# Optimization experiments

Measured on AMD Instinct MI355X. Metric: run time of the kernel, lower is better.

The kernel has to match this reference:

```python
import jax, jax.numpy as jnp
import numpy as np

C = 256
BN_EPS = 1e-5


def conv1x1(x, w, b):
    # x: (B, Cin, H, W), w: (Cout, Cin), b: (Cout,)
    return jnp.einsum('bchw,oc->bohw', x, w) + b[None, :, None, None]


def setup_inputs() -> dict:
    key = jax.random.key(0)
    ks = jax.random.split(key, 12)
    B, H, W = 8, 64, 64
    s = 1.0 / np.sqrt(C)
    inp = {
        'xi': jax.random.normal(ks[0], (B, C, H, W), jnp.float32),
        'xj': jax.random.normal(ks[1], (B, C, H, W), jnp.float32),
        'g_w': jax.random.normal(ks[2], (C, C), jnp.float32) * s,
        'g_b': jax.random.normal(ks[3], (C,), jnp.float32) * s,
        'theta_w': jax.random.normal(ks[4], (C, C), jnp.float32) * s,
        'theta_b': jax.random.normal(ks[5], (C,), jnp.float32) * s,
        'phi_w': jax.random.normal(ks[6], (C, C), jnp.float32) * s,
        'phi_b': jax.random.normal(ks[7], (C,), jnp.float32) * s,
        'W_w': jax.random.normal(ks[8], (C, C), jnp.float32) * s,
        'W_b': jax.random.normal(ks[9], (C,), jnp.float32) * s,
        'bn_gamma': jnp.ones((C,), jnp.float32),
        'bn_beta': jnp.zeros((C,), jnp.float32),
    }
    return inp


def reference(xi, xj, g_w, g_b, theta_w, theta_b, phi_w, phi_b, W_w, W_b, bn_gamma, bn_beta):
    B, Cc, H, W = xi.shape
    N = H * W
    # 1x1 conv projections, flattened to token sequences
    g_x = conv1x1(xj, g_w, g_b).reshape(B, Cc, N)        # (B, C, N)
    theta_x = conv1x1(xi, theta_w, theta_b).reshape(B, Cc, N)  # (B, C, N)
    phi_x = conv1x1(xj, phi_w, phi_b).reshape(B, Cc, N)  # (B, C, N)
    # f = theta^T @ phi, scaled by N (no softmax)
    f = jnp.einsum('bcn,bcm->bnm', theta_x, phi_x) / N   # (B, N, N)
    # y = f @ g^T, back to channel-first
    y = jnp.einsum('bnm,bcm->bcn', f, g_x).reshape(B, Cc, H, W)
    W_y = conv1x1(y, W_w, W_b)
    z = W_y + xi
    # BatchNorm2d (training-mode batch statistics, biased variance)
    mean = jnp.mean(z, axis=(0, 2, 3), keepdims=True)
    var = jnp.var(z, axis=(0, 2, 3), keepdims=True)
    z_hat = (z - mean) * jax.lax.rsqrt(var + BN_EPS)
    return z_hat * bn_gamma[None, :, None, None] + bn_beta[None, :, None, None]
```

## Files before the change

kernel.cpp:

```cpp
#include <hip/hip_runtime.h>
#include <cstddef>

#define CCH 256
#define NPIX 4096
#define NB 8
#define INVCNT (1.0f/32768.0f)
#define INVN (1.0f/4096.0f)

typedef __bf16 bf16_t;
typedef __attribute__((ext_vector_type(8))) __bf16 bf16x8;
typedef __attribute__((ext_vector_type(4))) __bf16 bf16x4;
typedef __attribute__((ext_vector_type(4))) float f32x4;

#define OFF_S      0u
#define OFF_AB     2048u
#define OFF_BMT    34816u
#define OFF_T1     67584u
#define OFF_R      67840u
#define OFF_W1     68096u
#define OFF_C1     68352u
#define OFF_G      68608u
#define OFF_MP     330752u
#define OFF_E      592896u
#define OFF_RSP    594944u
#define OFF_ZPS    627712u
#define OFF_ZPQ    758784u
#define OFF_SCALE  889856u
#define OFF_SHIFT  890112u
#define OFF_GP     890368u
#define OFF_XIT    5084672u

__device__ __forceinline__ void pack8(const float4& x, const float4& y, bf16x8& o) {
  o[0]=(bf16_t)x.x; o[1]=(bf16_t)x.y; o[2]=(bf16_t)x.z; o[3]=(bf16_t)x.w;
  o[4]=(bf16_t)y.x; o[5]=(bf16_t)y.y; o[6]=(bf16_t)y.z; o[7]=(bf16_t)y.w;
}

__device__ __forceinline__ void ld4(const float* p, float4& a0, float4& a1, float4& a2, float4& a3) {
  a0 = *(const float4*)p;       a1 = *(const float4*)(p + 4);
  a2 = *(const float4*)(p + 8); a3 = *(const float4*)(p + 12);
}

template <bool ATRANS>
__device__ __forceinline__ void mm64v(const float* __restrict__ A,
                                      const float* __restrict__ B,
                                      int i0, int j0,
                                      float (&acc)[2][4],
                                      float (*s1)[65], float (*s2)[65]) {
  const int t = threadIdx.x, tx = t & 15, ty = t >> 4;
  for (int k0 = 0; k0 < 256; k0 += 64) {
#pragma unroll
    for (int it = 0; it < 2; ++it) {
      const int f = t + 512 * it;
      const int row = f >> 4, cc = (f & 15) * 4;
      float4 va;
      if (ATRANS)
        va = *(const float4*)(A + (size_t)(k0 + row) * CCH + i0 + cc);
      else
        va = *(const float4*)(A + (size_t)(i0 + row) * CCH + k0 + cc);
      const float4 vb = *(const float4*)(B + (size_t)(k0 + row) * CCH + j0 + cc);
      s1[row][cc + 0] = va.x; s1[row][cc + 1] = va.y; s1[row][cc + 2] = va.z; s1[row][cc + 3] = va.w;
      s2[row][cc + 0] = vb.x; s2[row][cc + 1] = vb.y; s2[row][cc + 2] = vb.z; s2[row][cc + 3] = vb.w;
    }
    __syncthreads();
#pragma unroll 4
    for (int kk = 0; kk < 64; ++kk) {
      float ar[2], br[4];
#pragma unroll
      for (int i = 0; i < 2; ++i) ar[i] = ATRANS ? s1[kk][2 * ty + i] : s1[2 * ty + i][kk];
#pragma unroll
      for (int j = 0; j < 4; ++j) br[j] = s2[kk][4 * tx + j];
#pragma unroll
      for (int i = 0; i < 2; ++i)
#pragma unroll
        for (int j = 0; j < 4; ++j) acc[i][j] += ar[i] * br[j];
    }
    __syncthreads();
  }
}

__device__ void pre_body(int blk, const float* Ww, const float* gw, const float* phw,
                         const float* thw, const float* gb, const float* phb,
                         const float* thb, float* ws, unsigned char* SMEM) {
  const int t = threadIdx.x;
  if (blk < 32) {
    float (*s1)[65] = (float(*)[65])SMEM;
    float (*s2)[65] = (float(*)[65])(SMEM + 16640);
    const int tb = blk & 15;
    const int i0 = (tb >> 2) * 64, j0 = (tb & 3) * 64;
    float acc[2][4] = {};
    if (blk < 16) mm64v<false>(Ww, gw, i0, j0, acc, s1, s2);
    else          mm64v<true >(thw, phw, i0, j0, acc, s1, s2);
    bf16_t* outp = (bf16_t*)(ws + (blk < 16 ? OFF_AB : OFF_BMT));
    const int tx = t & 15, ty = t >> 4;
#pragma unroll
    for (int i = 0; i < 2; ++i) {
      bf16x4 mv;
#pragma unroll
      for (int q = 0; q < 4; ++q) mv[q] = (bf16_t)acc[i][q];
      *(bf16x4*)&outp[(size_t)(i0 + 2 * ty + i) * CCH + j0 + 4 * tx] = mv;
    }
  } else {
    if (t < 256) {
      float t1v = 0.f, rv = 0.f, w1v = 0.f;
      for (int k = 0; k < 256; ++k) {
        t1v += phw[k * CCH + t] * thb[k];
        rv  += thw[k * CCH + t] * phb[k];
        w1v += Ww[t * CCH + k] * gb[k];
      }
      ws[OFF_T1 + t] = t1v; ws[OFF_R + t] = rv; ws[OFF_W1 + t] = w1v;
    }
    float* red = (float*)SMEM;
    red[t] = (t < 256) ? phb[t] * thb[t] : 0.f;
    __syncthreads();
    for (int off = 256; off; off >>= 1) { if (t < off) red[t] += red[t + off]; __syncthreads(); }
    if (t == 0) ws[OFF_C1] = red[0];
  }
}

__device__ void cvtT_body(int bx, int b, const float* __restrict__ xi,
                          float* __restrict__ ws, unsigned char* SMEM) {
  bf16_t (*st)[72] = (bf16_t(*)[72])SMEM;
  const int c0 = (bx & 1) * 128;
  const int n0 = (bx >> 1) * 64;
  const float* X = xi + (size_t)b * CCH * NPIX;
  const int t = threadIdx.x;
  const int r = t >> 2, c4 = (t & 3) * 16;
  {
    float4 a0, a1, a2, a3;
    ld4(X + (size_t)(c0 + r) * NPIX + n0 + c4, a0, a1, a2, a3);
    bf16x8 u0, u1;
    pack8(a0, a1, u0); pack8(a2, a3, u1);
    *(bf16x8*)&st[r][c4] = u0;
    *(bf16x8*)&st[r][c4 + 8] = u1;
  }
  __syncthreads();
  bf16_t* Xit = (bf16_t*)(ws + OFF_XIT) + (size_t)b * NPIX * CCH;
  const int nr = t >> 3, cc = (t & 7) * 16;
  bf16x8 o0, o1;
#pragma unroll
  for (int j = 0; j < 8; ++j) o0[j] = st[cc + j][nr];
#pragma unroll
  for (int j = 0; j < 8; ++j) o1[j] = st[cc + 8 + j][nr];
  *(bf16x8*)(Xit + (size_t)(n0 + nr) * CCH + c0 + cc) = o0;
  *(bf16x8*)(Xit + (size_t)(n0 + nr) * CCH + c0 + cc + 8) = o1;
}

__device__ void gram_body(int ks, int b, const float* __restrict__ X,
                          float* __restrict__ ws, unsigned char* SMEM) {
  bf16_t (*sA)[256][40] = (bf16_t(*)[256][40])SMEM;
  const int t = threadIdx.x;
  const int w = t >> 6, lane = t & 63;
  const int wr = w >> 1, wc = w & 1;
  const int lr = lane & 15, hi = lane >> 4;
  const int fcol = 8 * hi;
  const f32x4 z4 = {0.f, 0.f, 0.f, 0.f};
  f32x4 acc[4][8];
#pragma unroll
  for (int fr = 0; fr < 4; ++fr)
#pragma unroll
    for (int fc = 0; fc < 8; ++fc) acc[fr][fc] = z4;
  float rsum = 0.f;
  const int k0 = ks * 256;
  const int srow = t >> 1, sh16 = (t & 1) * 16;

  float4 a0, a1, a2, a3;
  auto LOAD = [&](int kc) {
    ld4(X + (size_t)srow * NPIX + k0 + kc + sh16, a0, a1, a2, a3);
    rsum += a0.x + a0.y + a0.z + a0.w + a1.x + a1.y + a1.z + a1.w
          + a2.x + a2.y + a2.z + a2.w + a3.x + a3.y + a3.z + a3.w;
  };
  auto WRITE = [&](int q) {
    bf16x8 u0, u1;
    pack8(a0, a1, u0); pack8(a2, a3, u1);
    *(bf16x8*)&sA[q][srow][sh16] = u0;
    *(bf16x8*)&sA[q][srow][sh16 + 8] = u1;
  };

  LOAD(0);
  WRITE(0);
  __syncthreads();
  int cur = 0;
  for (int kc8 = 0; kc8 < 8; ++kc8) {
    if (kc8 < 7) LOAD(32 * (kc8 + 1));
    bf16x8 af[4];
#pragma unroll
    for (int fr = 0; fr < 4; ++fr)
      af[fr] = *(const bf16x8*)&sA[cur][64 * wr + 16 * fr + lr][fcol];
#pragma unroll
    for (int fc = 0; fc < 8; ++fc) {
      const bf16x8 bv = *(const bf16x8*)&sA[cur][128 * wc + 16 * fc + lr][fcol];
#pragma unroll
      for (int fr = 0; fr < 4; ++fr)
        acc[fr][fc] = __builtin_amdgcn_mfma_f32_16x16x32_bf16(af[fr], bv, acc[fr][fc], 0, 0, 0);
    }
    if (kc8 < 7) WRITE(cur ^ 1);
    __syncthreads();
    cur ^= 1;
  }

  {
    const float o = __shfl_down(rsum, 1);
    if (!(t & 1)) ws[OFF_RSP + ((size_t)(b * 16 + ks)) * CCH + srow] = rsum + o;
  }
  bf16_t* GPp = (bf16_t*)(ws + OFF_GP) + (size_t)(b * 16 + ks) * 65536;
  bf16_t (*sT)[264] = (bf16_t(*)[264])SMEM;
  const int rl = 16 * wr + 4 * hi;
#pragma unroll
  for (int fr = 0; fr < 4; ++fr) {
    __syncthreads();
#pragma unroll
    for (int fc = 0; fc < 8; ++fc)
#pragma unroll
      for (int reg = 0; reg < 4; ++reg)
        sT[rl + reg][128 * wc + 16 * fc + lr] = (bf16_t)acc[fr][fc][reg];
    __syncthreads();
    const int row = t >> 3;
    const int c32 = (t & 7) * 32;
    const int grow = 64 * (row >> 4) + 16 * fr + (row & 15);
#pragma unroll
    for (int q = 0; q < 4; ++q) {
      const bf16x8 v = *(const bf16x8*)&sT[row][c32 + 8 * q];
      *(bf16x8*)&GPp[(size_t)grow * CCH + c32 + 8 * q] = v;
    }
  }
}

__global__ __launch_bounds__(512) void k_mega(const float* __restrict__ xi,
                                              const float* __restrict__ xj,
                                              const float* __restrict__ Ww,
                                              const float* __restrict__ gw,
                                              const float* __restrict__ phw,
                                              const float* __restrict__ thw,
                                              const float* __restrict__ gb,
                                              const float* __restrict__ phb,
                                              const float* __restrict__ thb,
                                              float* __restrict__ ws) {
  __shared__ __align__(16) unsigned char SMEM[40960];
  const int bx = blockIdx.x, by = blockIdx.y;
  if (bx >= 144) {
    if (by == 0) pre_body(bx - 144, Ww, gw, phw, thw, gb, phb, thb, ws, SMEM);
    return;
  }
  if (bx >= 16) { cvtT_body(bx - 16, by, xi, ws, SMEM); return; }
  gram_body(bx, by, xj + (size_t)by * CCH * NPIX, ws, SMEM);
}

__global__ __launch_bounds__(256) void k_greduce(float* __restrict__ ws) {
  const int b = blockIdx.y, bx = blockIdx.x, t = threadIdx.x;
  const bf16_t* GPp = (const bf16_t*)(ws + OFF_GP) + (size_t)b * 16 * 65536;
  bf16_t* Gb = (bf16_t*)(ws + OFF_G) + (size_t)b * 65536;
  const int row = bx * 8 + (t >> 5);
  const int j8 = (t & 31) * 8;
  float s[8] = {};
#pragma unroll
  for (int ks = 0; ks < 16; ++ks) {
    const bf16x8 v = *(const bf16x8*)&GPp[(size_t)ks * 65536 + row * CCH + j8];
#pragma unroll
    for (int q = 0; q < 8; ++q) s[q] += (float)v[q];
  }
  bf16x8 o;
#pragma unroll
  for (int q = 0; q < 8; ++q) o[q] = (bf16_t)s[q];
  *(bf16x8*)&Gb[(size_t)row * CCH + j8] = o;
  if (t < 128) {
    const int rr = bx * 8 + (t >> 4), l = t & 15;
    float v = ws[OFF_RSP + ((size_t)(b * 16 + l)) * CCH + rr];
#pragma unroll
    for (int off = 8; off; off >>= 1) v += __shfl_down(v, off, 16);
    if (l == 0) ws[OFF_S + b * CCH + rr] = v;
  }
}

__global__ __launch_bounds__(256) void k_kmmat(const float* __restrict__ Wb, float* __restrict__ ws) {
  const int b = blockIdx.y;
  const int i0 = blockIdx.x * 32;
  const int t = threadIdx.x;
  const int w = t >> 6, lane = t & 63;
  const int rg = w >> 1, cg = w & 1;
  const int lr = lane & 15, hi = lane >> 4;
  const int fcol = 8 * hi;

  __shared__ __align__(16) bf16_t sA[2][32][40];
  __shared__ __align__(16) bf16_t sB[2][256][40];
  __shared__ __align__(16) bf16_t sK[32][264];
  __shared__ float sS[256], sT1[256], sR[256], sW1[256], sVS[256];
  __shared__ float sU[32];
  __shared__ float red[256];
  __shared__ float sdt_sh;

  const bf16_t* Ab  = (const bf16_t*)(ws + OFF_AB);
  const bf16_t* BmT = (const bf16_t*)(ws + OFF_BMT);
  const bf16_t* Gb  = (const bf16_t*)(ws + OFF_G) + (size_t)b * 65536;

  sS[t]  = ws[OFF_S + b * CCH + t];
  sT1[t] = ws[OFF_T1 + t];
  sR[t]  = ws[OFF_R + t];
  sW1[t] = ws[OFF_W1 + t];
  __syncthreads();
  red[t] = sS[t] * sT1[t];
  __syncthreads();
  for (int off = 128; off; off >>= 1) { if (t < off) red[t] += red[t + off]; __syncthreads(); }
  if (t == 0) sdt_sh = red[0];
  {
    float a = 0.f;
    for (int k8 = 0; k8 < 256; k8 += 8) {
      const bf16x8 v = *(const bf16x8*)&BmT[(size_t)t * CCH + k8];
#pragma unroll
      for (int q = 0; q < 8; ++q) a += (float)v[q] * sS[k8 + q];
    }
    sVS[t] = a;
  }
  if (t < 32) {
    float a = 0.f;
    for (int k8 = 0; k8 < 256; k8 += 8) {
      const bf16x8 v = *(const bf16x8*)&Ab[(size_t)(i0 + t) * CCH + k8];
#pragma unroll
      for (int q = 0; q < 8; ++q) a += (float)v[q] * sS[k8 + q];
    }
    sU[t] = a;
  }

  const f32x4 z4 = {0.f, 0.f, 0.f, 0.f};
  const int arow = t >> 2, achk = (t & 3) * 8;

  f32x4 acc[8];
#pragma unroll
  for (int fc = 0; fc < 8; ++fc) acc[fc] = z4;
  bf16x8 ra;
  bf16x8 gb8[4];
  auto LOADB = [&](int k) {
    if (t < 128) ra = *(const bf16x8*)&Ab[(size_t)(i0 + arow) * CCH + k + achk];
#pragma unroll
    for (int h = 0; h < 4; ++h)
      gb8[h] = *(const bf16x8*)&Gb[(size_t)(64 * h + arow) * CCH + k + achk];
  };
  auto WRITEB = [&](int q) {
    if (t < 128) *(bf16x8*)&sA[q][arow][achk] = ra;
#pragma unroll
    for (int h = 0; h < 4; ++h)
      *(bf16x8*)&sB[q][64 * h + arow][achk] = gb8[h];
  };
  LOADB(0);
  WRITEB(0);
  __syncthreads();
  int cur = 0;
  for (int ks = 0; ks < 8; ++ks) {
    if (ks < 7) LOADB(32 * (ks + 1));
    const bf16x8 af = *(const bf16x8*)&sA[cur][16 * rg + lr][fcol];
#pragma unroll
    for (int fc = 0; fc < 8; ++fc) {
      const bf16x8 bv = *(const bf16x8*)&sB[cur][128 * cg + 16 * fc + lr][fcol];
      acc[fc] = __builtin_amdgcn_mfma_f32_16x16x32_bf16(af, bv, acc[fc], 0, 0, 0);
    }
    if (ks < 7) WRITEB(cur ^ 1);
    __syncthreads();
    cur ^= 1;
  }
#pragma unroll
  for (int fc = 0; fc < 8; ++fc)
#pragma unroll
    for (int reg = 0; reg < 4; ++reg)
      sK[16 * rg + 4 * hi + reg][128 * cg + 16 * fc + lr] = (bf16_t)acc[fc][reg];
  __syncthreads();

  if (t < 32) {
    float dot = 0.f;
    for (int k8 = 0; k8 < 256; k8 += 8) {
      const bf16x8 v = *(const bf16x8*)&sK[t][k8];
#pragma unroll
      for (int q = 0; q < 8; ++q) dot += (float)v[q] * sT1[k8 + q];
    }
    const float c1 = ws[OFF_C1];
    const float ui = sU[t], w1i = sW1[i0 + t];
    ws[OFF_E + b * CCH + i0 + t] = INVN * (dot + c1 * ui + sdt_sh * w1i) + c1 * w1i + Wb[i0 + t];
  }

  f32x4 acc2[8];
#pragma unroll
  for (int fc = 0; fc < 8; ++fc) acc2[fc] = z4;
  bf16x8 rb[4];
  auto LOADC = [&](int k) {
#pragma unroll
    for (int h = 0; h < 4; ++h)
      rb[h] = *(const bf16x8*)&BmT[(size_t)(64 * h + arow) * CCH + k + achk];
  };
  auto WRITEC = [&](int q) {
#pragma unroll
    for (int h = 0; h < 4; ++h)
      *(bf16x8*)&sB[q][64 * h + arow][achk] = rb[h];
  };
  LOADC(0);
  WRITEC(0);
  __syncthreads();
  cur = 0;
  for (int ks = 0; ks < 8; ++ks) {
    if (ks < 7) LOADC(32 * (ks + 1));
    const bf16x8 af = *(const bf16x8*)&sK[16 * rg + lr][32 * ks + fcol];
#pragma unroll
    for (int fc = 0; fc < 8; ++fc) {
      const bf16x8 bv = *(const bf16x8*)&sB[cur][128 * cg + 16 * fc + lr][fcol];
      acc2[fc] = __builtin_amdgcn_mfma_f32_16x16x32_bf16(af, bv, acc2[fc], 0, 0, 0);
    }
    if (ks < 7) WRITEC(cur ^ 1);
    __syncthreads();
    cur ^= 1;
  }

  bf16_t* Mp = (bf16_t*)(ws + OFF_MP) + (size_t)b * 65536;
#pragma unroll
  for (int fc = 0; fc < 8; ++fc) {
    const int j = 128 * cg + 16 * fc + lr;
    const float rj = sR[j], vsj = sVS[j];
#pragma unroll
    for (int reg = 0; reg < 4; ++reg) {
      const int il = 16 * rg + 4 * hi + reg;
      const float ui = sU[il], w1i = sW1[i0 + il];
      float m = (acc2[fc][reg] + ui * rj + w1i * vsj) * INVN + w1i * rj;
      if (i0 + il == j) m += 1.0f;
      sK[16 * rg + 4 * hi + reg][128 * cg + 16 * fc + lr] = (bf16_t)m;
    }
  }
  __syncthreads();
  {
    const int row = t >> 3;
    const int c32 = (t & 7) * 32;
#pragma unroll
    for (int q = 0; q < 4; ++q) {
      const bf16x8 v = *(const bf16x8*)&sK[row][c32 + 8 * q];
      *(bf16x8*)&Mp[(size_t)(i0 + row) * CCH + c32 + 8 * q] = v;
    }
  }
}

template <int APPLY>
__global__ __launch_bounds__(256) void k_zmm(float* __restrict__ ws, float* __restrict__ out) {
  const int b = blockIdx.y, nblk = blockIdx.x;
  const int n0 = nblk * 64;
  const int t = threadIdx.x;
  const int w = t >> 6, lane = t & 63;
  const int rg = w >> 1, cg = w & 1;
  __shared__ __align__(16) bf16_t sA[2][64][40];
  __shared__ __align__(16) bf16_t sB[2][256][40];
  __shared__ float sC1[256], sC2[256];
  __shared__ float redS[4][128], redQ[4][128];
  {
    const float e = ws[OFF_E + b * CCH + t];
    if (APPLY) {
      const float sc = ws[OFF_SCALE + t];
      sC1[t] = sc;
      sC2[t] = e * sc + ws[OFF_SHIFT + t];
    } else {
      sC1[t] = e;
    }
  }
  const bf16_t* Xit = (const bf16_t*)(ws + OFF_XIT) + (size_t)b * NPIX * CCH;
  const bf16_t* Mp = (const bf16_t*)(ws + OFF_MP) + (size_t)b * 65536;
  const f32x4 z4 = {0.f, 0.f, 0.f, 0.f};
  f32x4 acc[2][8];
#pragma unroll
  for (int fr = 0; fr < 2; ++fr)
#pragma unroll
    for (int fc = 0; fc < 8; ++fc) acc[fr][fc] = z4;
  const int arow = t >> 2, achk = (t & 3) * 8;
  bf16x8 ra, rb0, rb1, rb2, rb3;
  ra  = *(const bf16x8*)(Xit + (size_t)(n0 + arow) * CCH + achk);
  rb0 = *(const bf16x8*)(Mp + (size_t)(arow)       * CCH + achk);
  rb1 = *(const bf16x8*)(Mp + (size_t)(64 + arow)  * CCH + achk);
  rb2 = *(const bf16x8*)(Mp + (size_t)(128 + arow) * CCH + achk);
  rb3 = *(const bf16x8*)(Mp + (size_t)(192 + arow) * CCH + achk);
  *(bf16x8*)&sA[0][arow][achk] = ra;
  *(bf16x8*)&sB[0][arow][achk] = rb0;
  *(bf16x8*)&sB[0][64 + arow][achk] = rb1;
  *(bf16x8*)&sB[0][128 + arow][achk] = rb2;
  *(bf16x8*)&sB[0][192 + arow][achk] = rb3;
  __syncthreads();
  int cur = 0;
  for (int ks = 0; ks < 8; ++ks) {
    const int nk = 32 * (ks + 1);
    if (ks < 7) {
      ra  = *(const bf16x8*)(Xit + (size_t)(n0 + arow) * CCH + nk + achk);
      rb0 = *(const bf16x8*)(Mp + (size_t)(arow)       * CCH + nk + achk);
      rb1 = *(const bf16x8*)(Mp + (size_t)(64 + arow)  * CCH + nk + achk);
      rb2 = *(const bf16x8*)(Mp + (size_t)(128 + arow) * CCH + nk + achk);
      rb3 = *(const bf16x8*)(Mp + (size_t)(192 + arow) * CCH + nk + achk);
    }
    const int fcol = 8 * (lane >> 4);
    const int lr = lane & 15;
    const bf16x8 af0 = *(const bf16x8*)&sA[cur][32 * rg + lr][fcol];
    const bf16x8 af1 = *(const bf16x8*)&sA[cur][32 * rg + 16 + lr][fcol];
#pragma unroll
    for (int fc = 0; fc < 8; ++fc) {
      const bf16x8 bv = *(const bf16x8*)&sB[cur][128 * cg + 16 * fc + lr][fcol];
      acc[0][fc] = __builtin_amdgcn_mfma_f32_16x16x32_bf16(af0, bv, acc[0][fc], 0, 0, 0);
      acc[1][fc] = __builtin_amdgcn_mfma_f32_16x16x32_bf16(af1, bv, acc[1][fc], 0, 0, 0);
    }
    if (ks < 7) {
      *(bf16x8*)&sA[cur ^ 1][arow][achk] = ra;
      *(bf16x8*)&sB[cur ^ 1][arow][achk] = rb0;
      *(bf16x8*)&sB[cur ^ 1][64 + arow][achk] = rb1;
      *(bf16x8*)&sB[cur ^ 1][128 + arow][achk] = rb2;
      *(bf16x8*)&sB[cur ^ 1][192 + arow][achk] = rb3;
    }
    __syncthreads();
    cur ^= 1;
  }
  if (APPLY) {
#pragma unroll
    for (int fc = 0; fc < 8; ++fc) {
      const int c = 128 * cg + 16 * fc + (lane & 15);
      const float sc = sC1[c], b2 = sC2[c];
      float* op = out + ((size_t)b * CCH + c) * NPIX + n0 + 32 * rg + ((lane >> 4) << 2);
#pragma unroll
      for (int fr = 0; fr < 2; ++fr) {
        float4 v;
        v.x = acc[fr][fc][0] * sc + b2;
        v.y = acc[fr][fc][1] * sc + b2;
        v.z = acc[fr][fc][2] * sc + b2;
        v.w = acc[fr][fc][3] * sc + b2;
        *(float4*)(op + 16 * fr) = v;
      }
    }
  } else {
    float ps[8], pq[8];
#pragma unroll
    for (int fc = 0; fc < 8; ++fc) {
      const int c = 128 * cg + 16 * fc + (lane & 15);
      const float e = sC1[c];
      float s = 0.f, q = 0.f;
#pragma unroll
      for (int fr = 0; fr < 2; ++fr)
#pragma unroll
        for (int reg = 0; reg < 4; ++reg) {
          const float z = acc[fr][fc][reg] + e;
          s += z; q += z * z;
        }
      s += __shfl_xor(s, 16); s += __shfl_xor(s, 32);
      q += __shfl_xor(q, 16); q += __shfl_xor(q, 32);
      ps[fc] = s; pq[fc] = q;
    }
    if (lane < 16) {
#pragma unroll
      for (int fc = 0; fc < 8; ++fc) {
        redS[w][16 * fc + lane] = ps[fc];
        redQ[w][16 * fc + lane] = pq[fc];
      }
    }
    __syncthreads();
    if (t < 256) {
      const int cg2 = t >> 7, c = t & 127;
      float s = 0.f, q = 0.f;
#pragma unroll
      for (int rg2 = 0; rg2 < 2; ++rg2) {
        s += redS[rg2 * 2 + cg2][c];
        q += redQ[rg2 * 2 + cg2][c];
      }
      ws[OFF_ZPS + (size_t)t * 512 + b * 64 + nblk] = s;
      ws[OFF_ZPQ + (size_t)t * 512 + b * 64 + nblk] = q;
    }
  }
}

__global__ __launch_bounds__(64) void k_bnstats(const float* __restrict__ gamma,
                                                const float* __restrict__ beta,
                                                float* __restrict__ ws) {
  const int c = blockIdx.x, t = threadIdx.x;
  const float* PS = ws + OFF_ZPS + (size_t)c * 512;
  const float* PQ = ws + OFF_ZPQ + (size_t)c * 512;
  float s = 0.f, q = 0.f;
#pragma unroll
  for (int e = 0; e < 8; ++e) { s += PS[t + 64 * e]; q += PQ[t + 64 * e]; }
#pragma unroll
  for (int off = 32; off; off >>= 1) { s += __shfl_down(s, off); q += __shfl_down(q, off); }
  if (t == 0) {
    const float mean = s * INVCNT;
    const float var = q * INVCNT - mean * mean;
    const float sc = gamma[c] * rsqrtf(var + 1e-5f);
    ws[OFF_SCALE + c] = sc;
    ws[OFF_SHIFT + c] = beta[c] - mean * sc;
  }
}

extern "C" void kernel_launch(void* const* d_in, const int* in_sizes, int n_in,
                              void* d_out, int out_size, void* d_ws, size_t ws_size,
                              hipStream_t stream) {
  const float* xi  = (const float*)d_in[0];
  const float* xj  = (const float*)d_in[1];
  const float* gw  = (const float*)d_in[2];
  const float* gb  = (const float*)d_in[3];
  const float* thw = (const float*)d_in[4];
  const float* thb = (const float*)d_in[5];
  const float* phw = (const float*)d_in[6];
  const float* phb = (const float*)d_in[7];
  const float* Ww  = (const float*)d_in[8];
  const float* Wb  = (const float*)d_in[9];
  const float* gamma = (const float*)d_in[10];
  const float* beta  = (const float*)d_in[11];
  float* ws = (float*)d_ws;
  float* out = (float*)d_out;

  k_mega<<<dim3(177, 8), 512, 0, stream>>>(xi, xj, Ww, gw, phw, thw, gb, phb, thb, ws);
  k_greduce<<<dim3(32, 8), 256, 0, stream>>>(ws);
  k_kmmat<<<dim3(8, 8), 256, 0, stream>>>(Wb, ws);
  k_zmm<0><<<dim3(64, 8), 256, 0, stream>>>(ws, out);
  k_bnstats<<<256, 64, 0, stream>>>(gamma, beta, ws);
  k_zmm<1><<<dim3(64, 8), 256, 0, stream>>>(ws, out);
}
```

Before: 88.23 us.

## Store z in bf16 once and apply BN from it; double gram split-K

The second z GEMM pass is replaced: the stats kernel now writes z (plus bias) to workspace in bf16 token-major layout, and a new lightweight apply kernel reads it back, transposes through shared memory and applies the BN scale and shift. This removes the recomputation of the whole z matmul. Separately, the gram kernel's split-K factor goes from 16 to 32 to add more blocks, which enlarges the partial buffer the reduce kernel must read. Storing z in bf16 adds rounding error plus an extra round trip through memory.

```diff
diff --git a/kernel.cpp b/kernel.cpp
--- a/kernel.cpp
+++ b/kernel.cpp
@@ -6,6 +6,7 @@
 #define NB 8
 #define INVCNT (1.0f/32768.0f)
 #define INVN (1.0f/4096.0f)
+#define NSPLIT 32
 
 typedef __bf16 bf16_t;
 typedef __attribute__((ext_vector_type(8))) __bf16 bf16x8;
@@ -23,12 +24,13 @@
 #define OFF_MP     330752u
 #define OFF_E      592896u
 #define OFF_RSP    594944u
-#define OFF_ZPS    627712u
-#define OFF_ZPQ    758784u
-#define OFF_SCALE  889856u
-#define OFF_SHIFT  890112u
-#define OFF_GP     890368u
-#define OFF_XIT    5084672u
+#define OFF_ZPS    660480u
+#define OFF_ZPQ    791552u
+#define OFF_SCALE  922624u
+#define OFF_SHIFT  922880u
+#define OFF_GP     923136u
+#define OFF_XIT    9311744u
+#define OFF_ZT     13506048u
 
 __device__ __forceinline__ void pack8(const float4& x, const float4& y, bf16x8& o) {
   o[0]=(bf16_t)x.x; o[1]=(bf16_t)x.y; o[2]=(bf16_t)x.z; o[3]=(bf16_t)x.w;
@@ -160,7 +162,7 @@
 #pragma unroll
     for (int fc = 0; fc < 8; ++fc) acc[fr][fc] = z4;
   float rsum = 0.f;
-  const int k0 = ks * 256;
+  const int k0 = ks * 128;
   const int srow = t >> 1, sh16 = (t & 1) * 16;
 
   float4 a0, a1, a2, a3;
@@ -180,8 +182,8 @@
   WRITE(0);
   __syncthreads();
   int cur = 0;
-  for (int kc8 = 0; kc8 < 8; ++kc8) {
-    if (kc8 < 7) LOAD(32 * (kc8 + 1));
+  for (int kc8 = 0; kc8 < 4; ++kc8) {
+    if (kc8 < 3) LOAD(32 * (kc8 + 1));
     bf16x8 af[4];
 #pragma unroll
     for (int fr = 0; fr < 4; ++fr)
@@ -193,16 +195,16 @@
       for (int fr = 0; fr < 4; ++fr)
         acc[fr][fc] = __builtin_amdgcn_mfma_f32_16x16x32_bf16(af[fr], bv, acc[fr][fc], 0, 0, 0);
     }
-    if (kc8 < 7) WRITE(cur ^ 1);
+    if (kc8 < 3) WRITE(cur ^ 1);
     __syncthreads();
     cur ^= 1;
   }
 
   {
     const float o = __shfl_down(rsum, 1);
-    if (!(t & 1)) ws[OFF_RSP + ((size_t)(b * 16 + ks)) * CCH + srow] = rsum + o;
-  }
-  bf16_t* GPp = (bf16_t*)(ws + OFF_GP) + (size_t)(b * 16 + ks) * 65536;
+    if (!(t & 1)) ws[OFF_RSP + ((size_t)(b * NSPLIT + ks)) * CCH + srow] = rsum + o;
+  }
+  bf16_t* GPp = (bf16_t*)(ws + OFF_GP) + (size_t)(b * NSPLIT + ks) * 65536;
   bf16_t (*sT)[264] = (bf16_t(*)[264])SMEM;
   const int rl = 16 * wr + 4 * hi;
 #pragma unroll
@@ -237,23 +239,23 @@
                                               float* __restrict__ ws) {
   __shared__ __align__(16) unsigned char SMEM[40960];
   const int bx = blockIdx.x, by = blockIdx.y;
-  if (bx >= 144) {
-    if (by == 0) pre_body(bx - 144, Ww, gw, phw, thw, gb, phb, thb, ws, SMEM);
+  if (bx >= 160) {
+    if (by == 0) pre_body(bx - 160, Ww, gw, phw, thw, gb, phb, thb, ws, SMEM);
     return;
   }
-  if (bx >= 16) { cvtT_body(bx - 16, by, xi, ws, SMEM); return; }
+  if (bx >= 32) { cvtT_body(bx - 32, by, xi, ws, SMEM); return; }
   gram_body(bx, by, xj + (size_t)by * CCH * NPIX, ws, SMEM);
 }
 
 __global__ __launch_bounds__(256) void k_greduce(float* __restrict__ ws) {
   const int b = blockIdx.y, bx = blockIdx.x, t = threadIdx.x;
-  const bf16_t* GPp = (const bf16_t*)(ws + OFF_GP) + (size_t)b * 16 * 65536;
+  const bf16_t* GPp = (const bf16_t*)(ws + OFF_GP) + (size_t)b * NSPLIT * 65536;
   bf16_t* Gb = (bf16_t*)(ws + OFF_G) + (size_t)b * 65536;
   const int row = bx * 8 + (t >> 5);
   const int j8 = (t & 31) * 8;
   float s[8] = {};
 #pragma unroll
-  for (int ks = 0; ks < 16; ++ks) {
+  for (int ks = 0; ks < NSPLIT; ++ks) {
     const bf16x8 v = *(const bf16x8*)&GPp[(size_t)ks * 65536 + row * CCH + j8];
 #pragma unroll
     for (int q = 0; q < 8; ++q) s[q] += (float)v[q];
@@ -262,11 +264,11 @@
 #pragma unroll
   for (int q = 0; q < 8; ++q) o[q] = (bf16_t)s[q];
   *(bf16x8*)&Gb[(size_t)row * CCH + j8] = o;
-  if (t < 128) {
-    const int rr = bx * 8 + (t >> 4), l = t & 15;
-    float v = ws[OFF_RSP + ((size_t)(b * 16 + l)) * CCH + rr];
-#pragma unroll
-    for (int off = 8; off; off >>= 1) v += __shfl_down(v, off, 16);
+  {
+    const int rr = bx * 8 + (t >> 5), l = t & 31;
+    float v = ws[OFF_RSP + ((size_t)(b * NSPLIT + l)) * CCH + rr];
+#pragma unroll
+    for (int off = 16; off; off >>= 1) v += __shfl_down(v, off, 32);
     if (l == 0) ws[OFF_S + b * CCH + rr] = v;
   }
 }
@@ -432,27 +434,20 @@
   }
 }
 
-template <int APPLY>
-__global__ __launch_bounds__(256) void k_zmm(float* __restrict__ ws, float* __restrict__ out) {
+__global__ __launch_bounds__(256) void k_zstat(float* __restrict__ ws) {
   const int b = blockIdx.y, nblk = blockIdx.x;
   const int n0 = nblk * 64;
   const int t = threadIdx.x;
   const int w = t >> 6, lane = t & 63;
   const int rg = w >> 1, cg = w & 1;
-  __shared__ __align__(16) bf16_t sA[2][64][40];
-  __shared__ __align__(16) bf16_t sB[2][256][40];
-  __shared__ float sC1[256], sC2[256];
+  const int lr = lane & 15, hi = lane >> 4;
+  __shared__ __align__(16) unsigned char ZSM[51200];
+  bf16_t (*sA)[64][40]  = (bf16_t(*)[64][40])ZSM;
+  bf16_t (*sB)[256][40] = (bf16_t(*)[256][40])(ZSM + 10240);
+  bf16_t (*sZm)[136]    = (bf16_t(*)[136])ZSM;
+  __shared__ float sE[256];
   __shared__ float redS[4][128], redQ[4][128];
-  {
-    const float e = ws[OFF_E + b * CCH + t];
-    if (APPLY) {
-      const float sc = ws[OFF_SCALE + t];
-      sC1[t] = sc;
-      sC2[t] = e * sc + ws[OFF_SHIFT + t];
-    } else {
-      sC1[t] = e;
-    }
-  }
+  sE[t] = ws[OFF_E + b * CCH + t];
   const bf16_t* Xit = (const bf16_t*)(ws + OFF_XIT) + (size_t)b * NPIX * CCH;
   const bf16_t* Mp = (const bf16_t*)(ws + OFF_MP) + (size_t)b * 65536;
   const f32x4 z4 = {0.f, 0.f, 0.f, 0.f};
@@ -484,8 +479,7 @@
       rb2 = *(const bf16x8*)(Mp + (size_t)(128 + arow) * CCH + nk + achk);
       rb3 = *(const bf16x8*)(Mp + (size_t)(192 + arow) * CCH + nk + achk);
     }
-    const int fcol = 8 * (lane >> 4);
-    const int lr = lane & 15;
+    const int fcol = 8 * hi;
     const bf16x8 af0 = *(const bf16x8*)&sA[cur][32 * rg + lr][fcol];
     const bf16x8 af1 = *(const bf16x8*)&sA[cur][32 * rg + 16 + lr][fcol];
 #pragma unroll
@@ -504,58 +498,63 @@
     __syncthreads();
     cur ^= 1;
   }
-  if (APPLY) {
+  float ps[8], pq[8];
+#pragma unroll
+  for (int fc = 0; fc < 8; ++fc) {
+    const int c = 128 * cg + 16 * fc + lr;
+    const float e = sE[c];
+    float s = 0.f, q = 0.f;
+#pragma unroll
+    for (int fr = 0; fr < 2; ++fr)
+#pragma unroll
+      for (int reg = 0; reg < 4; ++reg) {
+        const float z = acc[fr][fc][reg] + e;
+        s += z; q += z * z;
+      }
+    s += __shfl_xor(s, 16); s += __shfl_xor(s, 32);
+    q += __shfl_xor(q, 16); q += __shfl_xor(q, 32);
+    ps[fc] = s; pq[fc] = q;
+  }
+  if (lane < 16) {
 #pragma unroll
     for (int fc = 0; fc < 8; ++fc) {
-      const int c = 128 * cg + 16 * fc + (lane & 15);
-      const float sc = sC1[c], b2 = sC2[c];
-      float* op = out + ((size_t)b * CCH + c) * NPIX + n0 + 32 * rg + ((lane >> 4) << 2);
-#pragma unroll
-      for (int fr = 0; fr < 2; ++fr) {
-        float4 v;
-        v.x = acc[fr][fc][0] * sc + b2;
-        v.y = acc[fr][fc][1] * sc + b2;
-        v.z = acc[fr][fc][2] * sc + b2;
-        v.w = acc[fr][fc][3] * sc + b2;
-        *(float4*)(op + 16 * fr) = v;
+      redS[w][16 * fc + lane] = ps[fc];
+      redQ[w][16 * fc + lane] = pq[fc];
+    }
+  }
+  __syncthreads();
+  {
+    const int cg2 = t >> 7, c = t & 127;
+    float s = 0.f, q = 0.f;
+#pragma unroll
+    for (int rg2 = 0; rg2 < 2; ++rg2) {
+      s += redS[rg2 * 2 + cg2][c];
+      q += redQ[rg2 * 2 + cg2][c];
+    }
+    ws[OFF_ZPS + (size_t)t * 512 + b * 64 + nblk] = s;
+    ws[OFF_ZPQ + (size_t)t * 512 + b * 64 + nblk] = q;
+  }
+  bf16_t* ZT = (bf16_t*)(ws + OFF_ZT) + ((size_t)b * NPIX + n0) * CCH;
+  for (int h = 0; h < 2; ++h) {
+    __syncthreads();
+    if (cg == h) {
+#pragma unroll
+      for (int fc = 0; fc < 8; ++fc) {
+        const float e = sE[128 * h + 16 * fc + lr];
+#pragma unroll
+        for (int fr = 0; fr < 2; ++fr)
+#pragma unroll
+          for (int reg = 0; reg < 4; ++reg)
+            sZm[32 * rg + 16 * fr + 4 * hi + reg][16 * fc + lr] =
+                (bf16_t)(acc[fr][fc][reg] + e);
       }
     }
-  } else {
-    float ps[8], pq[8];
-#pragma unroll
-    for (int fc = 0; fc < 8; ++fc) {
-      const int c = 128 * cg + 16 * fc + (lane & 15);
-      const float e = sC1[c];
-      float s = 0.f, q = 0.f;
-#pragma unroll
-      for (int fr = 0; fr < 2; ++fr)
-#pragma unroll
-        for (int reg = 0; reg < 4; ++reg) {
-          const float z = acc[fr][fc][reg] + e;
-          s += z; q += z * z;
-        }
-      s += __shfl_xor(s, 16); s += __shfl_xor(s, 32);
-      q += __shfl_xor(q, 16); q += __shfl_xor(q, 32);
-      ps[fc] = s; pq[fc] = q;
-    }
-    if (lane < 16) {
-#pragma unroll
-      for (int fc = 0; fc < 8; ++fc) {
-        redS[w][16 * fc + lane] = ps[fc];
-        redQ[w][16 * fc + lane] = pq[fc];
-      }
-    }
-    __syncthreads();
-    if (t < 256) {
-      const int cg2 = t >> 7, c = t & 127;
-      float s = 0.f, q = 0.f;
-#pragma unroll
-      for (int rg2 = 0; rg2 < 2; ++rg2) {
-        s += redS[rg2 * 2 + cg2][c];
-        q += redQ[rg2 * 2 + cg2][c];
-      }
-      ws[OFF_ZPS + (size_t)t * 512 + b * 64 + nblk] = s;
-      ws[OFF_ZPQ + (size_t)t * 512 + b * 64 + nblk] = q;
+    __syncthreads();
+    const int row = t >> 2, cq = (t & 3) * 32;
+#pragma unroll
+    for (int q = 0; q < 4; ++q) {
+      const bf16x8 v = *(const bf16x8*)&sZm[row][cq + 8 * q];
+      *(bf16x8*)&ZT[(size_t)row * CCH + 128 * h + cq + 8 * q] = v;
     }
   }
 }
@@ -577,6 +576,37 @@
     const float sc = gamma[c] * rsqrtf(var + 1e-5f);
     ws[OFF_SCALE + c] = sc;
     ws[OFF_SHIFT + c] = beta[c] - mean * sc;
+  }
+}
+
+__global__ __launch_bounds__(256) void k_zapply(const float* __restrict__ ws,
+                                                float* __restrict__ out) {
+  const int b = blockIdx.y;
+  const int c0 = (blockIdx.x & 1) * 128;
+  const int n0 = (blockIdx.x >> 1) * 64;
+  __shared__ __align__(16) bf16_t sz[64][136];
+  const bf16_t* ZT = (const bf16_t*)(ws + OFF_ZT) + (size_t)b * NPIX * CCH;
+  const int t = threadIdx.x;
+  {
+    const int nr = t >> 2, cc = (t & 3) * 32;
+    const bf16_t* src = ZT + (size_t)(n0 + nr) * CCH + c0 + cc;
+#pragma unroll
+    for (int q = 0; q < 4; ++q)
+      *(bf16x8*)&sz[nr][cc + 8 * q] = *(const bf16x8*)(src + 8 * q);
+  }
+  __syncthreads();
+  const int c = t >> 1, half = t & 1;
+  const float sc = ws[OFF_SCALE + c0 + c];
+  const float sh = ws[OFF_SHIFT + c0 + c];
+  float* op = out + ((size_t)(b * CCH + c0 + c)) * NPIX + n0 + 32 * half;
+#pragma unroll
+  for (int q = 0; q < 8; ++q) {
+    float4 v;
+    v.x = (float)sz[32 * half + 4 * q + 0][c] * sc + sh;
+    v.y = (float)sz[32 * half + 4 * q + 1][c] * sc + sh;
+    v.z = (float)sz[32 * half + 4 * q + 2][c] * sc + sh;
+    v.w = (float)sz[32 * half + 4 * q + 3][c] * sc + sh;
+    *(float4*)(op + 4 * q) = v;
   }
 }
 
@@ -598,10 +628,10 @@
   float* ws = (float*)d_ws;
   float* out = (float*)d_out;
 
-  k_mega<<<dim3(177, 8), 512, 0, stream>>>(xi, xj, Ww, gw, phw, thw, gb, phb, thb, ws);
+  k_mega<<<dim3(193, 8), 512, 0, stream>>>(xi, xj, Ww, gw, phw, thw, gb, phb, thb, ws);
   k_greduce<<<dim3(32, 8), 256, 0, stream>>>(ws);
   k_kmmat<<<dim3(8, 8), 256, 0, stream>>>(Wb, ws);
-  k_zmm<0><<<dim3(64, 8), 256, 0, stream>>>(ws, out);
+  k_zstat<<<dim3(64, 8), 256, 0, stream>>>(ws);
   k_bnstats<<<256, 64, 0, stream>>>(gamma, beta, ws);
-  k_zmm<1><<<dim3(64, 8), 256, 0, stream>>>(ws, out);
-}
+  k_zapply<<<dim3(128, 8), 256, 0, stream>>>(ws, out);
+}
```

After: 102.1 us. 1.16x slower.

## Fuse BN-stat and apply GEMM passes into one cooperative kernel with grid sync

Applied to the files above, without the earlier changes.

Replaces the two GEMM passes plus the separate BN-stats kernel with a single cooperative kernel. It computes z once, accumulates the per-channel sum and sum of squares with atomics, does a grid-wide sync, then normalizes the accumulators still held in registers and writes the output. This drops the second GEMM over Xit/Mp and two kernel launches, at the cost of a grid barrier, atomic contention on 256 channels, and host-side occupancy queries on every call. If cooperative launch is unavailable it falls back to a two-kernel stat/apply path that also uses atomics.

```diff
diff --git a/kernel.cpp b/kernel.cpp
--- a/kernel.cpp
+++ b/kernel.cpp
@@ -1,5 +1,8 @@
 #include <hip/hip_runtime.h>
+#include <hip/hip_cooperative_groups.h>
 #include <cstddef>
+
+namespace cg = cooperative_groups;
 
 #define CCH 256
 #define NPIX 4096
@@ -23,10 +26,8 @@
 #define OFF_MP     330752u
 #define OFF_E      592896u
 #define OFF_RSP    594944u
-#define OFF_ZPS    627712u
-#define OFF_ZPQ    758784u
-#define OFF_SCALE  889856u
-#define OFF_SHIFT  890112u
+#define OFF_BSUM   627712u
+#define OFF_BSQ    627968u
 #define OFF_GP     890368u
 #define OFF_XIT    5084672u
 
@@ -276,7 +277,7 @@
   const int i0 = blockIdx.x * 32;
   const int t = threadIdx.x;
   const int w = t >> 6, lane = t & 63;
-  const int rg = w >> 1, cg = w & 1;
+  const int rg = w >> 1, cw = w & 1;
   const int lr = lane & 15, hi = lane >> 4;
   const int fcol = 8 * hi;
 
@@ -349,7 +350,7 @@
     const bf16x8 af = *(const bf16x8*)&sA[cur][16 * rg + lr][fcol];
 #pragma unroll
     for (int fc = 0; fc < 8; ++fc) {
-      const bf16x8 bv = *(const bf16x8*)&sB[cur][128 * cg + 16 * fc + lr][fcol];
+      const bf16x8 bv = *(const bf16x8*)&sB[cur][128 * cw + 16 * fc + lr][fcol];
       acc[fc] = __builtin_amdgcn_mfma_f32_16x16x32_bf16(af, bv, acc[fc], 0, 0, 0);
     }
     if (ks < 7) WRITEB(cur ^ 1);
@@ -360,7 +361,7 @@
   for (int fc = 0; fc < 8; ++fc)
 #pragma unroll
     for (int reg = 0; reg < 4; ++reg)
-      sK[16 * rg + 4 * hi + reg][128 * cg + 16 * fc + lr] = (bf16_t)acc[fc][reg];
+      sK[16 * rg + 4 * hi + reg][128 * cw + 16 * fc + lr] = (bf16_t)acc[fc][reg];
   __syncthreads();
 
   if (t < 32) {
@@ -398,7 +399,7 @@
     const bf16x8 af = *(const bf16x8*)&sK[16 * rg + lr][32 * ks + fcol];
 #pragma unroll
     for (int fc = 0; fc < 8; ++fc) {
-      const bf16x8 bv = *(const bf16x8*)&sB[cur][128 * cg + 16 * fc + lr][fcol];
+      const bf16x8 bv = *(const bf16x8*)&sB[cur][128 * cw + 16 * fc + lr][fcol];
       acc2[fc] = __builtin_amdgcn_mfma_f32_16x16x32_bf16(af, bv, acc2[fc], 0, 0, 0);
     }
     if (ks < 7) WRITEC(cur ^ 1);
@@ -409,7 +410,7 @@
   bf16_t* Mp = (bf16_t*)(ws + OFF_MP) + (size_t)b * 65536;
 #pragma unroll
   for (int fc = 0; fc < 8; ++fc) {
-    const int j = 128 * cg + 16 * fc + lr;
+    const int j = 128 * cw + 16 * fc + lr;
     const float rj = sR[j], vsj = sVS[j];
 #pragma unroll
     for (int reg = 0; reg < 4; ++reg) {
@@ -417,7 +418,7 @@
       const float ui = sU[il], w1i = sW1[i0 + il];
       float m = (acc2[fc][reg] + ui * rj + w1i * vsj) * INVN + w1i * rj;
       if (i0 + il == j) m += 1.0f;
-      sK[16 * rg + 4 * hi + reg][128 * cg + 16 * fc + lr] = (bf16_t)m;
+      sK[16 * rg + 4 * hi + reg][128 * cw + 16 * fc + lr] = (bf16_t)m;
     }
   }
   __syncthreads();
@@ -432,35 +433,16 @@
   }
 }
 
-template <int APPLY>
-__global__ __launch_bounds__(256) void k_zmm(float* __restrict__ ws, float* __restrict__ out) {
-  const int b = blockIdx.y, nblk = blockIdx.x;
-  const int n0 = nblk * 64;
-  const int t = threadIdx.x;
-  const int w = t >> 6, lane = t & 63;
-  const int rg = w >> 1, cg = w & 1;
-  __shared__ __align__(16) bf16_t sA[2][64][40];
-  __shared__ __align__(16) bf16_t sB[2][256][40];
-  __shared__ float sC1[256], sC2[256];
-  __shared__ float redS[4][128], redQ[4][128];
-  {
-    const float e = ws[OFF_E + b * CCH + t];
-    if (APPLY) {
-      const float sc = ws[OFF_SCALE + t];
-      sC1[t] = sc;
-      sC2[t] = e * sc + ws[OFF_SHIFT + t];
-    } else {
-      sC1[t] = e;
-    }
-  }
+__device__ __forceinline__ void zmm_core(const float* __restrict__ ws, int b, int n0,
+                                         f32x4 (&acc)[2][8],
+                                         bf16_t (*sA)[64][40], bf16_t (*sB)[256][40]) {
+  const int t = threadIdx.x;
+  const int lane = t & 63;
+  const int w = t >> 6;
+  const int rg = w >> 1, cw = w & 1;
+  const int lr = lane & 15, hi = lane >> 4;
   const bf16_t* Xit = (const bf16_t*)(ws + OFF_XIT) + (size_t)b * NPIX * CCH;
   const bf16_t* Mp = (const bf16_t*)(ws + OFF_MP) + (size_t)b * 65536;
-  const f32x4 z4 = {0.f, 0.f, 0.f, 0.f};
-  f32x4 acc[2][8];
-#pragma unroll
-  for (int fr = 0; fr < 2; ++fr)
-#pragma unroll
-    for (int fc = 0; fc < 8; ++fc) acc[fr][fc] = z4;
   const int arow = t >> 2, achk = (t & 3) * 8;
   bf16x8 ra, rb0, rb1, rb2, rb3;
   ra  = *(const bf16x8*)(Xit + (size_t)(n0 + arow) * CCH + achk);
@@ -484,13 +466,12 @@
       rb2 = *(const bf16x8*)(Mp + (size_t)(128 + arow) * CCH + nk + achk);
       rb3 = *(const bf16x8*)(Mp + (size_t)(192 + arow) * CCH + nk + achk);
     }
-    const int fcol = 8 * (lane >> 4);
-    const int lr = lane & 15;
+    const int fcol = 8 * hi;
     const bf16x8 af0 = *(const bf16x8*)&sA[cur][32 * rg + lr][fcol];
     const bf16x8 af1 = *(const bf16x8*)&sA[cur][32 * rg + 16 + lr][fcol];
 #pragma unroll
     for (int fc = 0; fc < 8; ++fc) {
-      const bf16x8 bv = *(const bf16x8*)&sB[cur][128 * cg + 16 * fc + lr][fcol];
+      const bf16x8 bv = *(const bf16x8*)&sB[cur][128 * cw + 16 * fc + lr][fcol];
       acc[0][fc] = __builtin_amdgcn_mfma_f32_16x16x32_bf16(af0, bv, acc[0][fc], 0, 0, 0);
       acc[1][fc] = __builtin_amdgcn_mfma_f32_16x16x32_bf16(af1, bv, acc[1][fc], 0, 0, 0);
     }
@@ -504,80 +485,153 @@
     __syncthreads();
     cur ^= 1;
   }
-  if (APPLY) {
+}
+
+__device__ __forceinline__ void bn_partials_atomic(float* __restrict__ ws, const float* sE,
+                                                   f32x4 (&acc)[2][8],
+                                                   float (*redS)[128], float (*redQ)[128]) {
+  const int t = threadIdx.x;
+  const int lane = t & 63, w = t >> 6;
+  const int cw = w & 1, lr = lane & 15;
+  float ps[8], pq[8];
+#pragma unroll
+  for (int fc = 0; fc < 8; ++fc) {
+    const int c = 128 * cw + 16 * fc + lr;
+    const float e = sE[c];
+    float s = 0.f, q = 0.f;
+#pragma unroll
+    for (int fr = 0; fr < 2; ++fr)
+#pragma unroll
+      for (int reg = 0; reg < 4; ++reg) {
+        const float z = acc[fr][fc][reg] + e;
+        s += z; q += z * z;
+      }
+    s += __shfl_xor(s, 16); s += __shfl_xor(s, 32);
+    q += __shfl_xor(q, 16); q += __shfl_xor(q, 32);
+    ps[fc] = s; pq[fc] = q;
+  }
+  if (lane < 16) {
 #pragma unroll
     for (int fc = 0; fc < 8; ++fc) {
-      const int c = 128 * cg + 16 * fc + (lane & 15);
-      const float sc = sC1[c], b2 = sC2[c];
-      float* op = out + ((size_t)b * CCH + c) * NPIX + n0 + 32 * rg + ((lane >> 4) << 2);
-#pragma unroll
-      for (int fr = 0; fr < 2; ++fr) {
-        float4 v;
-        v.x = acc[fr][fc][0] * sc + b2;
-        v.y = acc[fr][fc][1] * sc + b2;
-        v.z = acc[fr][fc][2] * sc + b2;
-        v.w = acc[fr][fc][3] * sc + b2;
-        *(float4*)(op + 16 * fr) = v;
-      }
-    }
-  } else {
-    float ps[8], pq[8];
-#pragma unroll
-    for (int fc = 0; fc < 8; ++fc) {
-      const int c = 128 * cg + 16 * fc + (lane & 15);
-      const float e = sC1[c];
-      float s = 0.f, q = 0.f;
-#pragma unroll
-      for (int fr = 0; fr < 2; ++fr)
-#pragma unroll
-        for (int reg = 0; reg < 4; ++reg) {
-          const float z = acc[fr][fc][reg] + e;
-          s += z; q += z * z;
-        }
-      s += __shfl_xor(s, 16); s += __shfl_xor(s, 32);
-      q += __shfl_xor(q, 16); q += __shfl_xor(q, 32);
-      ps[fc] = s; pq[fc] = q;
-    }
-    if (lane < 16) {
-#pragma unroll
-      for (int fc = 0; fc < 8; ++fc) {
-        redS[w][16 * fc + lane] = ps[fc];
-        redQ[w][16 * fc + lane] = pq[fc];
-      }
-    }
-    __syncthreads();
-    if (t < 256) {
-      const int cg2 = t >> 7, c = t & 127;
-      float s = 0.f, q = 0.f;
-#pragma unroll
-      for (int rg2 = 0; rg2 < 2; ++rg2) {
-        s += redS[rg2 * 2 + cg2][c];
-        q += redQ[rg2 * 2 + cg2][c];
-      }
-      ws[OFF_ZPS + (size_t)t * 512 + b * 64 + nblk] = s;
-      ws[OFF_ZPQ + (size_t)t * 512 + b * 64 + nblk] = q;
-    }
-  }
-}
-
-__global__ __launch_bounds__(64) void k_bnstats(const float* __restrict__ gamma,
-                                                const float* __restrict__ beta,
-                                                float* __restrict__ ws) {
-  const int c = blockIdx.x, t = threadIdx.x;
-  const float* PS = ws + OFF_ZPS + (size_t)c * 512;
-  const float* PQ = ws + OFF_ZPQ + (size_t)c * 512;
-  float s = 0.f, q = 0.f;
-#pragma unroll
-  for (int e = 0; e < 8; ++e) { s += PS[t + 64 * e]; q += PQ[t + 64 * e]; }
-#pragma unroll
-  for (int off = 32; off; off >>= 1) { s += __shfl_down(s, off); q += __shfl_down(q, off); }
-  if (t == 0) {
-    const float mean = s * INVCNT;
-    const float var = q * INVCNT - mean * mean;
-    const float sc = gamma[c] * rsqrtf(var + 1e-5f);
-    ws[OFF_SCALE + c] = sc;
-    ws[OFF_SHIFT + c] = beta[c] - mean * sc;
-  }
+      redS[w][16 * fc + lane] = ps[fc];
+      redQ[w][16 * fc + lane] = pq[fc];
+    }
+  }
+  __syncthreads();
+  {
+    const int cg2 = t >> 7, c = t & 127;
+    float s = 0.f, q = 0.f;
+#pragma unroll
+    for (int rg2 = 0; rg2 < 2; ++rg2) {
+      s += redS[rg2 * 2 + cg2][c];
+      q += redQ[rg2 * 2 + cg2][c];
+    }
+    atomicAdd(&ws[OFF_BSUM + t], s);
+    atomicAdd(&ws[OFF_BSQ + t], q);
+  }
+}
+
+__device__ __forceinline__ void z_apply(const float* sC1, const float* sC2,
+                                        f32x4 (&acc)[2][8],
+                                        float* __restrict__ out, int b, int n0) {
+  const int t = threadIdx.x;
+  const int lane = t & 63, w = t >> 6;
+  const int rg = w >> 1, cw = w & 1;
+  const int lr = lane & 15, hi = lane >> 4;
+#pragma unroll
+  for (int fc = 0; fc < 8; ++fc) {
+    const int c = 128 * cw + 16 * fc + lr;
+    const float sc = sC1[c], b2 = sC2[c];
+    float* op = out + ((size_t)b * CCH + c) * NPIX + n0 + 32 * rg + 4 * hi;
+#pragma unroll
+    for (int fr = 0; fr < 2; ++fr) {
+      float4 v;
+      v.x = acc[fr][fc][0] * sc + b2;
+      v.y = acc[fr][fc][1] * sc + b2;
+      v.z = acc[fr][fc][2] * sc + b2;
+      v.w = acc[fr][fc][3] * sc + b2;
+      *(float4*)(op + 16 * fr) = v;
+    }
+  }
+}
+
+__global__ __launch_bounds__(256) void k_zstat(float* __restrict__ ws) {
+  const int b = blockIdx.y, n0 = blockIdx.x * 64;
+  const int t = threadIdx.x;
+  __shared__ __align__(16) bf16_t sA[2][64][40];
+  __shared__ __align__(16) bf16_t sB[2][256][40];
+  __shared__ float sE[256];
+  __shared__ float redS[4][128], redQ[4][128];
+  sE[t] = ws[OFF_E + b * CCH + t];
+  const f32x4 z4 = {0.f, 0.f, 0.f, 0.f};
+  f32x4 acc[2][8];
+#pragma unroll
+  for (int fr = 0; fr < 2; ++fr)
+#pragma unroll
+    for (int fc = 0; fc < 8; ++fc) acc[fr][fc] = z4;
+  zmm_core(ws, b, n0, acc, sA, sB);
+  bn_partials_atomic(ws, sE, acc, redS, redQ);
+}
+
+__global__ __launch_bounds__(256) void k_zapply(float* __restrict__ ws, float* __restrict__ out,
+                                                const float* __restrict__ gamma,
+                                                const float* __restrict__ beta) {
+  const int b = blockIdx.y, n0 = blockIdx.x * 64;
+  const int t = threadIdx.x;
+  __shared__ __align__(16) bf16_t sA[2][64][40];
+  __shared__ __align__(16) bf16_t sB[2][256][40];
+  __shared__ float sC1[256], sC2[256];
+  {
+    const float e = ws[OFF_E + b * CCH + t];
+    const float sv = ws[OFF_BSUM + t], qv = ws[OFF_BSQ + t];
+    const float mean = sv * INVCNT;
+    const float var = qv * INVCNT - mean * mean;
+    const float sc = gamma[t] * rsqrtf(var + 1e-5f);
+    sC1[t] = sc;
+    sC2[t] = e * sc + beta[t] - mean * sc;
+  }
+  const f32x4 z4 = {0.f, 0.f, 0.f, 0.f};
+  f32x4 acc[2][8];
+#pragma unroll
+  for (int fr = 0; fr < 2; ++fr)
+#pragma unroll
+    for (int fc = 0; fc < 8; ++fc) acc[fr][fc] = z4;
+  zmm_core(ws, b, n0, acc, sA, sB);
+  z_apply(sC1, sC2, acc, out, b, n0);
+}
+
+__global__ __launch_bounds__(256, 2) void k_zfused(float* __restrict__ ws,
+                                                   float* __restrict__ out,
+                                                   const float* __restrict__ gamma,
+                                                   const float* __restrict__ beta) {
+  const int bid = blockIdx.x;
+  const int b = bid >> 6, n0 = (bid & 63) * 64;
+  const int t = threadIdx.x;
+  __shared__ __align__(16) bf16_t sA[2][64][40];
+  __shared__ __align__(16) bf16_t sB[2][256][40];
+  __shared__ float sE[256];
+  __shared__ float sC1[256], sC2[256];
+  __shared__ float redS[4][128], redQ[4][128];
+  sE[t] = ws[OFF_E + b * CCH + t];
+  const f32x4 z4 = {0.f, 0.f, 0.f, 0.f};
+  f32x4 acc[2][8];
+#pragma unroll
+  for (int fr = 0; fr < 2; ++fr)
+#pragma unroll
+    for (int fc = 0; fc < 8; ++fc) acc[fr][fc] = z4;
+  zmm_core(ws, b, n0, acc, sA, sB);
+  bn_partials_atomic(ws, sE, acc, redS, redQ);
+  cg::this_grid().sync();
+  {
+    const float sv = ws[OFF_BSUM + t], qv = ws[OFF_BSQ + t];
+    const float mean = sv * INVCNT;
+    const float var = qv * INVCNT - mean * mean;
+    const float sc = gamma[t] * rsqrtf(var + 1e-5f);
+    sC1[t] = sc;
+    sC2[t] = sE[t] * sc + beta[t] - mean * sc;
+  }
+  __syncthreads();
+  z_apply(sC1, sC2, acc, out, b, n0);
 }
 
 extern "C" void kernel_launch(void* const* d_in, const int* in_sizes, int n_in,
@@ -601,7 +655,29 @@
   k_mega<<<dim3(177, 8), 512, 0, stream>>>(xi, xj, Ww, gw, phw, thw, gb, phb, thb, ws);
   k_greduce<<<dim3(32, 8), 256, 0, stream>>>(ws);
   k_kmmat<<<dim3(8, 8), 256, 0, stream>>>(Wb, ws);
-  k_zmm<0><<<dim3(64, 8), 256, 0, stream>>>(ws, out);
-  k_bnstats<<<256, 64, 0, stream>>>(gamma, beta, ws);
-  k_zmm<1><<<dim3(64, 8), 256, 0, stream>>>(ws, out);
-}
+  hipMemsetAsync(ws + OFF_BSUM, 0, 512 * sizeof(float), stream);
+
+  int dev = 0;
+  hipGetDevice(&dev);
+  int coopAttr = 0;
+  hipDeviceGetAttribute(&coopAttr, hipDeviceAttributeCooperativeLaunch, dev);
+  int maxb = 0;
+  if (coopAttr)
+    hipOccupancyMaxActiveBlocksPerMultiprocessor(&maxb, k_zfused, 256, 0);
+
+  bool done = false;
+  if (coopAttr && maxb >= 2) {
+    float* wsp = ws;
+    float* outp = out;
+    const float* gammap = gamma;
+    const float* betap = beta;
+    void* args[] = {(void*)&wsp, (void*)&outp, (void*)&gammap, (void*)&betap};
+    hipError_t err = hipLaunchCooperativeKernel((void*)k_zfused, dim3(512), dim3(256),
+                                                args, 0, stream);
+    done = (err == hipSuccess);
+  }
+  if (!done) {
+    k_zstat<<<dim3(64, 8), 256, 0, stream>>>(ws);
+    k_zapply<<<dim3(64, 8), 256, 0, stream>>>(ws, out, gamma, beta);
+  }
+}
```

Result: slower. 96.30 us (+9.2%).
